# Optimization experiments

Hardware: AMD Instinct MI355X
Metric: run time of the kernel (lower is better)

The kernel has to match this reference:

```python
import jax, jax.numpy as jnp
import numpy as np

B, N, D = 512, 500000, 128
K = 100


def setup_inputs() -> dict:
    key = jax.random.key(0)
    kq, kc = jax.random.split(key)
    queries = jax.random.normal(kq, (B, D), dtype=jnp.float32)
    candidates = jax.random.normal(kc, (N, D), dtype=jnp.float32)
    identifiers = jnp.arange(N, dtype=jnp.int32)
    return {
        "queries": queries,
        "candidates": candidates,
        "identifiers": identifiers,
        "num_candidates": K,
    }


def reference(queries, candidates, identifiers, num_candidates):
    # scores: [B, N] dense similarity matrix (dot product)
    scores = jnp.einsum("bd,nd->bn", queries, candidates)
    # top-k per query row
    values, indices = jax.lax.top_k(scores, num_candidates)  # [B, K] each
    top_ids = jnp.take(identifiers, indices, axis=0)          # [B, K]
    return values, top_ids
```

## Files before the change

kernel.cpp:

```cpp
#include <hip/hip_runtime.h>
#include <cfloat>


#define D_DIM 128
#define K_TOP 100
#define THRESH_SIGMA 3.25f
#define CAP_MAX 512
#define KEEP_MAXF 256
#define FGRID 512
#define TROWS 64

typedef short bf16x8 __attribute__((ext_vector_type(8)));
typedef float f32x4 __attribute__((ext_vector_type(4)));

__device__ __forceinline__ unsigned short f2bf(float x) {
    unsigned u = __float_as_uint(x);
    return (unsigned short)((u + 0x7FFFu + ((u >> 16) & 1u)) >> 16);
}

__device__ __forceinline__ unsigned long long make_key(float v, unsigned id) {
    unsigned vb = __float_as_uint(v);
    unsigned vm = (vb & 0x80000000u) ? ~vb : (vb | 0x80000000u);
    return ((unsigned long long)vm << 32) | (0xFFFFFFFFu - id);
}

template <int S>
__device__ inline void bitonic_sort_u64(unsigned long long* buf) {
    for (int k = 2; k <= S; k <<= 1) {
        for (int j = k >> 1; j > 0; j >>= 1) {
            __syncthreads();
            for (int i = threadIdx.x; i < S; i += blockDim.x) {
                int l = i ^ j;
                if (l > i) {
                    unsigned long long a = buf[i], b = buf[l];
                    bool sw = ((i & k) == 0) ? (a > b) : (a < b);
                    if (sw) { buf[i] = b; buf[l] = a; }
                }
            }
        }
    }
    __syncthreads();
}

__global__ void prep2_kernel(const float* __restrict__ Qm, float* __restrict__ thr,
                             int* __restrict__ cnt, int B) {
    int b = blockIdx.x * blockDim.x + threadIdx.x;
    if (b >= B) return;
    float s = 0.f;
    for (int d = 0; d < D_DIM; ++d) { float v = Qm[(size_t)b * D_DIM + d]; s = fmaf(v, v, s); }
    thr[b] = THRESH_SIGMA * sqrtf(s);
    cnt[b] = 0;
}

__global__ void qfrag_kernel(const float* __restrict__ Qm, uint4* __restrict__ qf,
                             int B, int nch) {
    int tid = blockIdx.x * blockDim.x + threadIdx.x;
    int total = nch * 8 * 4 * 64;
    if (tid >= total) return;
    int l  = tid & 63;
    int ks = (tid >> 6) & 3;
    int qb = (tid >> 8) & 7;
    int qch = tid >> 11;
    int qrow = qch * 128 + qb * 16 + (l & 15);
    int k0 = ks * 32 + (l >> 4) * 8;
    uint4 o = make_uint4(0u, 0u, 0u, 0u);
    if (qrow < B) {
        const float* src = Qm + (size_t)qrow * D_DIM + k0;
        unsigned r[4];
#pragma unroll
        for (int j = 0; j < 4; ++j)
            r[j] = (unsigned)f2bf(src[2 * j]) | ((unsigned)f2bf(src[2 * j + 1]) << 16);
        o = make_uint4(r[0], r[1], r[2], r[3]);
    }
    qf[tid] = o;
}

__global__ __launch_bounds__(512, 4) void mfma_filter_kernel(
    const float* __restrict__ cand, const bf16x8* __restrict__ qfrag,
    const float* __restrict__ thr, unsigned* __restrict__ idbuf,
    int* __restrict__ cnt, int N, int Bg, int cap, int nch, int ntiles) {
    __shared__ __align__(16) char cl[2][TROWS * 512];
    const int t = threadIdx.x;
    const int w = t >> 6;
    const int l = t & 63;

    const bool qv = ((w >> 1) < nch);
    const int qch = qv ? (w >> 1) : (nch > 0 ? nch - 1 : 0);
    const int qb0 = (w & 1) * 4;
    bf16x8 bq[4][4];
#pragma unroll
    for (int qb = 0; qb < 4; ++qb)
#pragma unroll
        for (int ks = 0; ks < 4; ++ks)
            bq[qb][ks] = qfrag[((qch * 8 + qb0 + qb) * 4 + ks) * 64 + l];
    float tvq[4];
#pragma unroll
    for (int qb = 0; qb < 4; ++qb) {
        int qg = qch * 128 + (qb0 + qb) * 16 + (l & 15);
        tvq[qb] = (qv && qg < Bg) ? thr[qg] : 3.0e38f;
    }

    int tile = blockIdx.x;
    if (tile >= ntiles) return;

#define STAGE(BUFI, T)                                                              \
    do {                                                                            \
        int c0s = (T) * TROWS;                                                      \
        _Pragma("unroll")                                                           \
        for (int i = 0; i < 4; ++i) {                                               \
            int rl = (w * 4 + i) * 2 + (l >> 5);                                    \
            int gr = c0s + rl; if (gr > N - 1) gr = N - 1;                          \
            int ug = (l & 31) ^ (rl & 7);                                           \
            const float* srcp = cand + (size_t)gr * D_DIM + ug * 4;                 \
            __builtin_amdgcn_global_load_lds(                                       \
                (const __attribute__((address_space(1))) void*)srcp,                \
                (__attribute__((address_space(3))) void*)(&cl[BUFI][(w * 4 + i) * 1024]), \
                16, 0, 0);                                                          \
        }                                                                           \
    } while (0)

    STAGE(0, tile);
    int cur = 0;
#pragma unroll 1
    while (true) {
        int nxt = tile + FGRID;
        bool hn = (nxt < ntiles);
        if (hn) {
            STAGE(cur ^ 1, nxt);
            asm volatile("s_waitcnt vmcnt(4)" ::: "memory");
        } else {
            asm volatile("s_waitcnt vmcnt(0)" ::: "memory");
        }
        __builtin_amdgcn_s_barrier();

        {
            const char* bp = cl[cur];
            int c0 = tile * TROWS;
#pragma unroll
            for (int cb = 0; cb < 4; ++cb) {
                int r = cb * 16 + (l & 15);
                int sb = r * 512, s = r & 7;
                bf16x8 af[4];
#pragma unroll
                for (int ks = 0; ks < 4; ++ks) {
                    int u0 = ks * 8 + (l >> 4) * 2;
                    f32x4 f0 = *reinterpret_cast<const f32x4*>(bp + sb + ((u0 ^ s) << 4));
                    f32x4 f1 = *reinterpret_cast<const f32x4*>(bp + sb + (((u0 + 1) ^ s) << 4));
                    union { bf16x8 v; unsigned u[4]; } p;
                    p.u[0] = (__float_as_uint(f0[0]) >> 16) | (__float_as_uint(f0[1]) & 0xFFFF0000u);
                    p.u[1] = (__float_as_uint(f0[2]) >> 16) | (__float_as_uint(f0[3]) & 0xFFFF0000u);
                    p.u[2] = (__float_as_uint(f1[0]) >> 16) | (__float_as_uint(f1[1]) & 0xFFFF0000u);
                    p.u[3] = (__float_as_uint(f1[2]) >> 16) | (__float_as_uint(f1[3]) & 0xFFFF0000u);
                    af[ks] = p.v;
                }
                f32x4 acc[4];
#pragma unroll
                for (int qb = 0; qb < 4; ++qb) acc[qb] = (f32x4){0.f, 0.f, 0.f, 0.f};
#pragma unroll
                for (int ks = 0; ks < 4; ++ks) {
                    bf16x8 a = af[ks];
#pragma unroll
                    for (int qb = 0; qb < 4; ++qb)
                        acc[qb] = __builtin_amdgcn_mfma_f32_16x16x32_bf16(
                            a, bq[qb][ks], acc[qb], 0, 0, 0);
                }
#pragma unroll
                for (int qb = 0; qb < 4; ++qb) {
                    float tv = tvq[qb];
                    f32x4 a = acc[qb];
                    float m = fmaxf(fmaxf(a[0], a[1]), fmaxf(a[2], a[3]));
                    if (m > tv) {
                        int qg = qch * 128 + (qb0 + qb) * 16 + (l & 15);
#pragma unroll
                        for (int rr = 0; rr < 4; ++rr) {
                            if (a[rr] > tv) {
                                int cid = c0 + cb * 16 + ((l >> 4) << 2) + rr;
                                if (cid < N) {
                                    int pos = atomicAdd(&cnt[qg], 1);
                                    if (pos < cap) idbuf[(size_t)qg * cap + pos] = (unsigned)cid;
                                }
                            }
                        }
                    }
                }
            }
        }

        if (!hn) break;
        __builtin_amdgcn_s_barrier();
        cur ^= 1; tile = nxt;
    }
#undef STAGE
}

__global__ void fallback_kernel(const float* __restrict__ Qm, const float* __restrict__ cand,
                                unsigned* __restrict__ idbuf, int* __restrict__ cnt,
                                int N, int cap) {
    int q = blockIdx.x;
    int c0 = cnt[q];
    if (c0 >= K_TOP && c0 <= cap) return;
    int keep = (cap < KEEP_MAXF) ? cap : KEEP_MAXF;

    __shared__ unsigned long long buf[2048];
    __shared__ float qrow[D_DIM];
    __shared__ int bn;
    __shared__ float theta;
    __shared__ int validn;
    for (int i = threadIdx.x; i < D_DIM; i += blockDim.x) qrow[i] = Qm[(size_t)q * D_DIM + i];
    for (int i = threadIdx.x; i < 2048; i += blockDim.x) buf[i] = 0ULL;
    if (threadIdx.x == 0) { bn = 0; theta = -3.0e38f; }
    __syncthreads();

    for (int base = 0; base < N; base += blockDim.x) {
        int c = base + threadIdx.x;
        if (c < N) {
            float s = 0.f;
            for (int d = 0; d < D_DIM; ++d) s = fmaf(qrow[d], cand[(size_t)c * D_DIM + d], s);
            if (s > theta) {
                int p = atomicAdd(&bn, 1);
                if (p < 2048) buf[p] = make_key(s, (unsigned)c);
            }
        }
        __syncthreads();
        if (bn > 2048 - 256 - 8) {
            bitonic_sort_u64<2048>(buf);
            unsigned long long kv = (threadIdx.x < (unsigned)keep) ? buf[2047 - threadIdx.x] : 0ULL;
            __syncthreads();
            for (int i = threadIdx.x; i < 2048; i += blockDim.x) buf[i] = 0ULL;
            __syncthreads();
            if (threadIdx.x < (unsigned)keep) buf[threadIdx.x] = kv;
            if ((int)threadIdx.x == keep - 1) {
                unsigned vm = (unsigned)(kv >> 32);
                unsigned vb = (vm & 0x80000000u) ? (vm ^ 0x80000000u) : ~vm;
                theta = __uint_as_float(vb) - 0.01f;
            }
            if (threadIdx.x == 0) bn = keep;
            __syncthreads();
        }
    }
    bitonic_sort_u64<2048>(buf);
    if (threadIdx.x == 0) validn = 0;
    __syncthreads();
    unsigned long long kv = (threadIdx.x < (unsigned)keep) ? buf[2047 - threadIdx.x] : 0ULL;
    if (kv != 0ULL) atomicAdd(&validn, 1);
    __syncthreads();
    if ((int)threadIdx.x < validn && threadIdx.x < (unsigned)keep) {
        unsigned id = 0xFFFFFFFFu - (unsigned)(kv & 0xFFFFFFFFu);
        if (id < (unsigned)N) idbuf[(size_t)q * cap + threadIdx.x] = id;
    }
    if (threadIdx.x == 0) cnt[q] = (validn < keep) ? validn : keep;
}

__device__ __forceinline__ float np_lane_chain(float q0, float b0v, float q1, float b1v,
                                               float q2, float b2v, float q3, float b3v,
                                               float acc) {
    float t = __fadd_rn(__fmul_rn(q3, b3v), acc);
    t = __fadd_rn(__fmul_rn(q2, b2v), t);
    t = __fadd_rn(__fmul_rn(q1, b1v), t);
    return __fadd_rn(__fmul_rn(q0, b0v), t);
}

__device__ __forceinline__ float np_score(const float* __restrict__ qrow,
                                          const float* __restrict__ crow) {
    float acc0 = 0.f, acc1 = 0.f, acc2 = 0.f, acc3 = 0.f;
#pragma unroll
    for (int d0 = 0; d0 < D_DIM; d0 += 16) {
        float4 b0 = *reinterpret_cast<const float4*>(crow + d0 + 0);
        float4 b1 = *reinterpret_cast<const float4*>(crow + d0 + 4);
        float4 b2 = *reinterpret_cast<const float4*>(crow + d0 + 8);
        float4 b3 = *reinterpret_cast<const float4*>(crow + d0 + 12);
        acc0 = np_lane_chain(qrow[d0 + 0], b0.x, qrow[d0 + 4], b1.x,
                             qrow[d0 + 8], b2.x, qrow[d0 + 12], b3.x, acc0);
        acc1 = np_lane_chain(qrow[d0 + 1], b0.y, qrow[d0 + 5], b1.y,
                             qrow[d0 + 9], b2.y, qrow[d0 + 13], b3.y, acc1);
        acc2 = np_lane_chain(qrow[d0 + 2], b0.z, qrow[d0 + 6], b1.z,
                             qrow[d0 + 10], b2.z, qrow[d0 + 14], b3.z, acc2);
        acc3 = np_lane_chain(qrow[d0 + 3], b0.w, qrow[d0 + 7], b1.w,
                             qrow[d0 + 11], b2.w, qrow[d0 + 15], b3.w, acc3);
    }
    return __fadd_rn(__fadd_rn(acc0, acc1), __fadd_rn(acc2, acc3));
}

__global__ __launch_bounds__(256) void select_kernel(
    const float* __restrict__ Qm, const float* __restrict__ cand,
    const unsigned* __restrict__ idbuf, const int* __restrict__ cnt,
    const int* __restrict__ ident, float* __restrict__ out, int N, int B, int cap) {
    __shared__ unsigned long long skey[CAP_MAX];
    __shared__ float qrow[D_DIM];
    int q = blockIdx.x;
    for (int i = threadIdx.x; i < D_DIM; i += blockDim.x) qrow[i] = Qm[(size_t)q * D_DIM + i];
    __syncthreads();

    int n = cnt[q]; if (n > cap) n = cap; if (n > CAP_MAX) n = CAP_MAX;
    for (int i = threadIdx.x; i < CAP_MAX; i += blockDim.x) {
        unsigned long long key = 0ULL;
        if (i < n) {
            unsigned id = idbuf[(size_t)q * cap + i];
            if (id < (unsigned)N) {
                float s = np_score(qrow, cand + (size_t)id * D_DIM);
                key = make_key(s, id);
            }
        }
        skey[i] = key;
    }

    bitonic_sort_u64<CAP_MAX>(skey);

    for (int t = threadIdx.x; t < K_TOP; t += blockDim.x) {
        unsigned long long key = skey[CAP_MAX - 1 - t];
        unsigned vm = (unsigned)(key >> 32);
        unsigned vb = (vm & 0x80000000u) ? (vm ^ 0x80000000u) : ~vm;
        unsigned id = 0xFFFFFFFFu - (unsigned)(key & 0xFFFFFFFFu);
        if (id >= (unsigned)N) id = 0;
        out[(size_t)q * K_TOP + t] = __uint_as_float(vb);
        out[(size_t)B * K_TOP + (size_t)q * K_TOP + t] = (float)ident[id];
    }
}

extern "C" void kernel_launch(void* const* d_in, const int* in_sizes, int n_in,
                              void* d_out, int out_size, void* d_ws, size_t ws_size,
                              hipStream_t stream) {
    const float* queries = (const float*)d_in[0];
    const float* cands   = (const float*)d_in[1];
    const int*   ident   = (const int*)d_in[2];
    const int B = in_sizes[0] / D_DIM;
    const int N = in_sizes[2];
    float* out = (float*)d_out;
    const int nch = (B + 127) >> 7;
    const int ntiles = (N + TROWS - 1) / TROWS;

    char* ws = (char*)d_ws;
    int*   cnt = (int*)ws;
    float* thr = (float*)(ws + 2048);
    uint4* qfrag = (uint4*)(ws + 4096);
    size_t ids_off = 4096 + (size_t)nch * 32768;
    unsigned* idbuf = (unsigned*)(ws + ids_off);
    int cap = CAP_MAX;
    if (ws_size > ids_off) {
        size_t fit = (ws_size - ids_off) / ((size_t)B * 4);
        if (fit < (size_t)cap) cap = (int)fit;
    } else cap = 1;
    if (cap < 1) cap = 1;

    prep2_kernel<<<(B + 255) / 256, 256, 0, stream>>>(queries, thr, cnt, B);
    int qft = nch * 2048;
    qfrag_kernel<<<(qft + 255) / 256, 256, 0, stream>>>(queries, qfrag, B, nch);

    int ngrp = (nch + 3) / 4;
    for (int g = 0; g < ngrp; ++g) {
        int nch_g = nch - g * 4; if (nch_g > 4) nch_g = 4;
        int B_g = B - g * 512; if (B_g > 512) B_g = 512;
        mfma_filter_kernel<<<FGRID, 512, 0, stream>>>(
            cands, (const bf16x8*)(qfrag + (size_t)g * 8192),
            thr + (size_t)g * 512, idbuf + (size_t)g * 512 * cap,
            cnt + (size_t)g * 512, N, B_g, cap, nch_g, ntiles);
    }

    fallback_kernel<<<B, 256, 0, stream>>>(queries, cands, idbuf, cnt, N, cap);

    select_kernel<<<B, 256, 0, stream>>>(queries, cands, idbuf, cnt, ident, out, N, B, cap);
}
```

Before: 191.3 us.

## Stage candidate tiles through registers as bf16 instead of direct global-to-LDS fp32

```diff
diff --git a/kernel.cpp b/kernel.cpp
--- a/kernel.cpp
+++ b/kernel.cpp
@@ -79,7 +79,7 @@
     const float* __restrict__ cand, const bf16x8* __restrict__ qfrag,
     const float* __restrict__ thr, unsigned* __restrict__ idbuf,
     int* __restrict__ cnt, int N, int Bg, int cap, int nch, int ntiles) {
-    __shared__ __align__(16) char cl[2][TROWS * 512];
+    __shared__ __align__(16) char cl[2][TROWS * 256];
     const int t = threadIdx.x;
     const int w = t >> 6;
     const int l = t & 63;
@@ -103,35 +103,39 @@
     int tile = blockIdx.x;
     if (tile >= ntiles) return;
 
-#define STAGE(BUFI, T)                                                              \
-    do {                                                                            \
-        int c0s = (T) * TROWS;                                                      \
-        _Pragma("unroll")                                                           \
-        for (int i = 0; i < 4; ++i) {                                               \
-            int rl = (w * 4 + i) * 2 + (l >> 5);                                    \
-            int gr = c0s + rl; if (gr > N - 1) gr = N - 1;                          \
-            int ug = (l & 31) ^ (rl & 7);                                           \
-            const float* srcp = cand + (size_t)gr * D_DIM + ug * 4;                 \
-            __builtin_amdgcn_global_load_lds(                                       \
-                (const __attribute__((address_space(1))) void*)srcp,                \
-                (__attribute__((address_space(3))) void*)(&cl[BUFI][(w * 4 + i) * 1024]), \
-                16, 0, 0);                                                          \
-        }                                                                           \
-    } while (0)
-
-    STAGE(0, tile);
+    const int srow = t >> 3;
+    const int scol = (t & 7) * 16;
+    float4 v[4];
+
+    auto load_tile = [&](int ti) {
+        int gr = ti * TROWS + srow; if (gr > N - 1) gr = N - 1;
+        const float4* src = reinterpret_cast<const float4*>(cand + (size_t)gr * D_DIM + scol);
+        v[0] = src[0]; v[1] = src[1]; v[2] = src[2]; v[3] = src[3];
+    };
+    auto write_tile = [&](int bufi) {
+        unsigned u[8];
+#pragma unroll
+        for (int j = 0; j < 4; ++j) {
+            u[2 * j]     = (__float_as_uint(v[j].x) >> 16) | (__float_as_uint(v[j].y) & 0xFFFF0000u);
+            u[2 * j + 1] = (__float_as_uint(v[j].z) >> 16) | (__float_as_uint(v[j].w) & 0xFFFF0000u);
+        }
+        int u0 = (t & 7) * 2, s = srow & 7;
+        *reinterpret_cast<uint4*>(&cl[bufi][srow * 256 + ((u0 ^ s) << 4)]) =
+            make_uint4(u[0], u[1], u[2], u[3]);
+        *reinterpret_cast<uint4*>(&cl[bufi][srow * 256 + (((u0 + 1) ^ s) << 4)]) =
+            make_uint4(u[4], u[5], u[6], u[7]);
+    };
+
+    load_tile(tile);
+    write_tile(0);
+    __syncthreads();
+
     int cur = 0;
 #pragma unroll 1
     while (true) {
         int nxt = tile + FGRID;
         bool hn = (nxt < ntiles);
-        if (hn) {
-            STAGE(cur ^ 1, nxt);
-            asm volatile("s_waitcnt vmcnt(4)" ::: "memory");
-        } else {
-            asm volatile("s_waitcnt vmcnt(0)" ::: "memory");
-        }
-        __builtin_amdgcn_s_barrier();
+        if (hn) load_tile(nxt);
 
         {
             const char* bp = cl[cur];
@@ -139,20 +143,12 @@
 #pragma unroll
             for (int cb = 0; cb < 4; ++cb) {
                 int r = cb * 16 + (l & 15);
-                int sb = r * 512, s = r & 7;
+                int sb = r * 256, s = r & 7;
                 bf16x8 af[4];
 #pragma unroll
-                for (int ks = 0; ks < 4; ++ks) {
-                    int u0 = ks * 8 + (l >> 4) * 2;
-                    f32x4 f0 = *reinterpret_cast<const f32x4*>(bp + sb + ((u0 ^ s) << 4));
-                    f32x4 f1 = *reinterpret_cast<const f32x4*>(bp + sb + (((u0 + 1) ^ s) << 4));
-                    union { bf16x8 v; unsigned u[4]; } p;
-                    p.u[0] = (__float_as_uint(f0[0]) >> 16) | (__float_as_uint(f0[1]) & 0xFFFF0000u);
-                    p.u[1] = (__float_as_uint(f0[2]) >> 16) | (__float_as_uint(f0[3]) & 0xFFFF0000u);
-                    p.u[2] = (__float_as_uint(f1[0]) >> 16) | (__float_as_uint(f1[1]) & 0xFFFF0000u);
-                    p.u[3] = (__float_as_uint(f1[2]) >> 16) | (__float_as_uint(f1[3]) & 0xFFFF0000u);
-                    af[ks] = p.v;
-                }
+                for (int ks = 0; ks < 4; ++ks)
+                    af[ks] = *reinterpret_cast<const bf16x8*>(
+                        bp + sb + (((ks * 4 + (l >> 4)) ^ s) << 4));
                 f32x4 acc[4];
 #pragma unroll
                 for (int qb = 0; qb < 4; ++qb) acc[qb] = (f32x4){0.f, 0.f, 0.f, 0.f};
@@ -187,10 +183,10 @@
         }
 
         if (!hn) break;
-        __builtin_amdgcn_s_barrier();
+        write_tile(cur ^ 1);
+        __syncthreads();
         cur ^= 1; tile = nxt;
     }
-#undef STAGE
 }
 
 __global__ void fallback_kernel(const float* __restrict__ Qm, const float* __restrict__ cand,
```

After: 205.2 us. 1.07x slower.
